# Kernel optimization log

Hardware: AMD Instinct MI355X
Metric: run time of the kernel (lower is better)

Reference implementation:

```python
import jax, jax.numpy as jnp
import numpy as np


def softmax_kernel(data, projection, is_query, eps=1e-4):
    # data: [b,h,n,d], projection: [m,d]
    d = data.shape[-1]
    data_normalizer = d ** -0.25
    ratio = projection.shape[0] ** -0.5
    data_dash = jnp.einsum('bhnd,md->bhnm', data_normalizer * data, projection)
    diag_data = (data ** 2).sum(axis=-1) * 0.5 * (data_normalizer ** 2)  # [b,h,n]
    diag_data = diag_data[..., None]
    if is_query:
        m = jnp.max(data_dash, axis=-1, keepdims=True)  # per-query max
    else:
        m = jnp.max(data_dash)  # global max over all keys
    return ratio * (jnp.exp(data_dash - diag_data - m) + eps)


def linear_attention(q, k, v):
    # q,k: [b,h,n,m] feature maps; v: [b,h,n,e]
    D_inv = 1.0 / jnp.einsum('bhnm,bhm->bhn', q, k.sum(axis=-2))
    context = jnp.einsum('bhnm,bhne->bhme', k, v)
    return jnp.einsum('bhme,bhnm,bhn->bhne', context, q, D_inv)


def setup_inputs() -> dict:
    key = jax.random.key(0)
    k1, k2, k3, k4 = jax.random.split(key, 4)
    B, H, N, D, M = 4, 16, 4096, 64, 256
    # gaussian orthogonal random matrix (scaling=0): 4 orthogonal DxD blocks,
    # rows rescaled by norms of gaussian rows
    blocks = []
    kk = k4
    for _ in range(M // D):
        kk, sub = jax.random.split(kk)
        g = jax.random.normal(sub, (D, D), dtype=jnp.float32)
        qmat, _ = jnp.linalg.qr(g)
        blocks.append(qmat.T)
    final = jnp.concatenate(blocks, axis=0)  # [M, D]
    kk, sub = jax.random.split(kk)
    multiplier = jnp.linalg.norm(jax.random.normal(sub, (M, D), dtype=jnp.float32), axis=1)
    proj = multiplier[:, None] * final
    return {
        'q': jax.random.normal(k1, (B, H, N, D), dtype=jnp.float32),
        'k': jax.random.normal(k2, (B, H, N, D), dtype=jnp.float32),
        'v': jax.random.normal(k3, (B, H, N, D), dtype=jnp.float32),
        'projection': proj,
    }


def reference(q, k, v, projection):
    q_prime = softmax_kernel(q, projection, is_query=True)
    k_prime = softmax_kernel(k, projection, is_query=False)
    return linear_attention(q_prime, k_prime, v)
```

## Files before the change

### kernel.cpp

```cpp
#include <hip/hip_runtime.h>
#include <hip/hip_bf16.h>


#define BH    64
#define NSEQ  4096
#define DD    64
#define MM    256
#define DN    0.35355339059327373f
#define RATIO 0.0625f
#define EPS   1e-4f
#define NSEG  8

#define CTX_OFF  0
#define KSUM_OFF (BH*MM*DD)
#define VSUM_OFF (KSUM_OFF + BH*MM)
#define MG_OFF   (VSUM_OFF + BH*DD)
#define CTX_SLICE (BH*MM*DD)

typedef __attribute__((ext_vector_type(8)))  short bf16x8;
typedef __attribute__((ext_vector_type(16))) float f32x16;

#define MFMA(a,b,c) __builtin_amdgcn_mfma_f32_32x32x16_bf16((a),(b),(c),0,0,0)
#define PATROW(r,h) ((((r)&3) + 8*((r)>>2)) + 4*(h))

__device__ __forceinline__ unsigned pkbf(float lo, float hi) {
    union { __hip_bfloat162 b2; unsigned u; } cvt;
    cvt.b2 = __float22bfloat162_rn(make_float2(lo, hi));
    return cvt.u;
}
__device__ __forceinline__ bf16x8 hi8(const float* x) {
    union { unsigned w[4]; bf16x8 v; } r;
    r.w[0] = pkbf(x[0], x[1]);
    r.w[1] = pkbf(x[2], x[3]);
    r.w[2] = pkbf(x[4], x[5]);
    r.w[3] = pkbf(x[6], x[7]);
    return r.v;
}
__device__ __forceinline__ unsigned short f2bf(float x) {
    unsigned u = __float_as_uint(x);
    return (unsigned short)((u + 0x7fffu + ((u >> 16) & 1u)) >> 16);
}
__device__ __forceinline__ unsigned ford(float f) {
    unsigned u = __float_as_uint(f);
    return (u & 0x80000000u) ? ~u : (u | 0x80000000u);
}
__device__ __forceinline__ float ford_inv(unsigned u) {
    return (u & 0x80000000u) ? __uint_as_float(u & 0x7fffffffu) : __uint_as_float(~u);
}
template<int BASE>
__device__ __forceinline__ bf16x8 repack8(const f32x16& a, int h) {
    unsigned X0 = pkbf(a[BASE+0], a[BASE+1]);
    unsigned X1 = pkbf(a[BASE+2], a[BASE+3]);
    unsigned Y0 = pkbf(a[BASE+4], a[BASE+5]);
    unsigned Y1 = pkbf(a[BASE+6], a[BASE+7]);
    unsigned tX0 = (unsigned)__shfl_xor((int)X0, 32);
    unsigned tX1 = (unsigned)__shfl_xor((int)X1, 32);
    unsigned tY0 = (unsigned)__shfl_xor((int)Y0, 32);
    unsigned tY1 = (unsigned)__shfl_xor((int)Y1, 32);
    union { unsigned w[4]; bf16x8 v; } r;
    r.w[0] = h ? tY0 : X0;
    r.w[1] = h ? tY1 : X1;
    r.w[2] = h ? Y0 : tX0;
    r.w[3] = h ? Y1 : tX1;
    return r.v;
}

__global__ __launch_bounds__(512, 2)
void keys_kernel(const float* __restrict__ kg, const float* __restrict__ vg,
                 const float* __restrict__ pg, float* __restrict__ ws,
                 float* __restrict__ outp)
{
    __shared__ __align__(16) short kf[2][64*64];
    __shared__ __align__(16) short vT[2][64*64];
    __shared__ float diagl[2][64];
    __shared__ float vswr[8][64];

    const int tid  = threadIdx.x;
    const int wv   = tid >> 6;
    const int lane = tid & 63;
    const int l31  = lane & 31;
    const int h    = lane >> 5;
    const int bh   = blockIdx.x >> 3;
    const int seg  = blockIdx.x & 7;

    const int kn = tid >> 3, kdg = tid & 7;
    const int ve = tid & 63, vnr = tid >> 6;

    bf16x8 pBh[4];
    {
        const int m = 32*wv + l31;
#pragma unroll
        for (int ks = 0; ks < 4; ++ks) {
            const int d0 = 16*ks + 8*h;
            float x[8];
            *(float4*)&x[0] = *(const float4*)(pg + m*64 + d0);
            *(float4*)&x[4] = *(const float4*)(pg + m*64 + d0 + 4);
#pragma unroll
            for (int i = 0; i < 8; ++i) x[i] *= DN;
            pBh[ks] = hi8(x);
        }
    }

    f32x16 cacc0, cacc1;
#pragma unroll
    for (int i = 0; i < 16; ++i) { cacc0[i] = 0.f; cacc1[i] = 0.f; }
    float ksacc = 0.f, mloc = -3e38f, vsacc = 0.f;

    float kx[8], vx[8];

    auto loads = [&](int ch) {
        const size_t kb = ((size_t)(bh*NSEQ + seg*512 + ch*64 + kn)) * 64 + kdg*8;
        *(float4*)&kx[0] = *(const float4*)(kg + kb);
        *(float4*)&kx[4] = *(const float4*)(kg + kb + 4);
        const size_t vb = ((size_t)(bh*NSEQ + seg*512 + ch*64 + vnr*8)) * 64 + ve;
#pragma unroll
        for (int j = 0; j < 8; ++j) vx[j] = vg[vb + (size_t)j*64];
    };

    auto stage_write = [&](int b) {
        float ss = 0.f;
#pragma unroll
        for (int i = 0; i < 8; ++i) ss = fmaf(kx[i], kx[i], ss);
        ss += __shfl_xor(ss, 1); ss += __shfl_xor(ss, 2); ss += __shfl_xor(ss, 4);
        if (kdg == 0) diagl[b][kn] = ss * 0.0625f;
        *(bf16x8*)&kf[b][kdg*512 + ((kn*8) ^ (kdg*8))] = hi8(kx);
#pragma unroll
        for (int j = 0; j < 8; ++j) vsacc += vx[j];
        *(bf16x8*)&vT[b][ve*64 + ((vnr*8) ^ (8*(ve & 7)))] = hi8(vx);
    };

    auto sgemm = [&](int b, f32x16& r0, f32x16& r1) {
#pragma unroll
        for (int i = 0; i < 16; ++i) { r0[i] = 0.f; r1[i] = 0.f; }
#pragma unroll
        for (int ks = 0; ks < 4; ++ks) {
            const int dg = ks*2 + h;
            const int ofs = dg*512 + ((l31*8) ^ (dg*8));
            bf16x8 a0 = *(const bf16x8*)&kf[b][ofs];
            bf16x8 a1 = *(const bf16x8*)&kf[b][ofs + 256];
            r0 = MFMA(a0, pBh[ks], r0);
            r1 = MFMA(a1, pBh[ks], r1);
        }
    };

    loads(0);
    stage_write(0);
    __syncthreads();

    for (int ch = 0; ch < 8; ++ch) {
        const int bc = ch & 1, bn = bc ^ 1;
        if (ch < 7) loads(ch + 1);

        f32x16 s0, s1;
        __builtin_amdgcn_s_setprio(1);
        sgemm(bc, s0, s1);
        __builtin_amdgcn_s_setprio(0);

        {
            float kp = 0.f;
#pragma unroll
            for (int g = 0; g < 4; ++g) {
                const float4 dq0 = *(const float4*)&diagl[bc][8*g + 4*h];
                const float4 dq1 = *(const float4*)&diagl[bc][32 + 8*g + 4*h];
                const float d0[4] = {dq0.x, dq0.y, dq0.z, dq0.w};
                const float d1[4] = {dq1.x, dq1.y, dq1.z, dq1.w};
#pragma unroll
                for (int j = 0; j < 4; ++j) {
                    const int r = 4*g + j;
                    mloc = fmaxf(mloc, s0[r]);
                    const float w0 = __expf(s0[r] - d0[j]);
                    s0[r] = w0; kp += w0;
                    mloc = fmaxf(mloc, s1[r]);
                    const float w1 = __expf(s1[r] - d1[j]);
                    s1[r] = w1; kp += w1;
                }
            }
            ksacc += kp;
        }
        bf16x8 wfr[4];
        wfr[0] = repack8<0>(s0, h);
        wfr[1] = repack8<8>(s0, h);
        wfr[2] = repack8<0>(s1, h);
        wfr[3] = repack8<8>(s1, h);

        __builtin_amdgcn_s_setprio(1);
#pragma unroll
        for (int ks = 0; ks < 4; ++ks) {
            const int nb = 16*ks + 8*h;
            const int sw = 8*(l31 & 7);
            bf16x8 b0 = *(const bf16x8*)&vT[bc][l31*64      + (nb ^ sw)];
            bf16x8 b1 = *(const bf16x8*)&vT[bc][(l31+32)*64 + (nb ^ sw)];
            cacc0 = MFMA(wfr[ks], b0, cacc0);
            cacc1 = MFMA(wfr[ks], b1, cacc1);
        }
        __builtin_amdgcn_s_setprio(0);

        if (ch < 7) stage_write(bn);
        __syncthreads();
    }

    ksacc += __shfl_xor(ksacc, 32);
    if (h == 0) atomicAdd(&ws[KSUM_OFF + bh*MM + 32*wv + l31], ksacc);

#pragma unroll
    for (int m = 1; m <= 32; m <<= 1) mloc = fmaxf(mloc, __shfl_xor(mloc, m));
    if (lane == 0) atomicMax((unsigned*)&ws[MG_OFF], ford(mloc));

    {
        float* cb = outp + (size_t)(seg*BH + bh) * (MM*DD);
#pragma unroll
        for (int r = 0; r < 16; ++r) {
            const int m = 32*wv + PATROW(r, h);
            cb[m*64 + l31]      = cacc0[r];
            cb[m*64 + l31 + 32] = cacc1[r];
        }
    }

    vswr[wv][lane] = vsacc;
    __syncthreads();
    if (tid < 64) {
        float s = 0.f;
#pragma unroll
        for (int w = 0; w < 8; ++w) s += vswr[w][tid];
        atomicAdd(&ws[VSUM_OFF + bh*DD + tid], s);
    }
}

__global__ __launch_bounds__(512)
void reduce_kernel(const float* __restrict__ outp, float* __restrict__ ws)
{
    const int idx = blockIdx.x * 512 + threadIdx.x;
    const float4* o4 = (const float4*)outp;
    float4 s = o4[idx];
#pragma unroll
    for (int sl = 1; sl < NSEG; ++sl) {
        float4 t = o4[sl*(CTX_SLICE/4) + idx];
        s.x += t.x; s.y += t.y; s.z += t.z; s.w += t.w;
    }
    ((float4*)(ws + CTX_OFF))[idx] = s;
}

__global__ __launch_bounds__(512, 2)
void query_kernel(const float* __restrict__ qg, const float* __restrict__ pg,
                  const float* __restrict__ ws, float* __restrict__ out)
{
    __shared__ __align__(16) short pfh[MM*DD];
    __shared__ __align__(16) short ctxb[32*64*8];
    __shared__ float ksuml[MM];
    __shared__ float ctxsuml[DD];
    __shared__ float ksumsuml;
    __shared__ float epsl[8][32];
    __shared__ float denl[8][32];

    const int tid  = threadIdx.x;
    const int wv   = tid >> 6;
    const int lane = tid & 63;
    const int l31  = lane & 31;
    const int h    = lane >> 5;
    const int bh   = blockIdx.x >> 3;
    const int seg  = blockIdx.x & 7;

    const float mg = ford_inv(*(const unsigned*)&ws[MG_OFF]);
    const float cs = RATIO * __expf(-mg);
    const float ce = RATIO * EPS;

    if (tid < DD) ctxsuml[tid] = 0.f;
    if (tid == 0) ksumsuml = 0.f;
    __syncthreads();

    {
        const int m = tid >> 1, dh = tid & 1;
#pragma unroll
        for (int b = 0; b < 4; ++b) {
            const int d0 = dh*32 + b*8;
            float x[8];
            *(float4*)&x[0] = *(const float4*)(pg + m*64 + d0);
            *(float4*)&x[4] = *(const float4*)(pg + m*64 + d0 + 4);
#pragma unroll
            for (int i = 0; i < 8; ++i) x[i] *= DN;
            const int g = ((m>>5)*4 + (d0>>4))*2 + ((d0>>3)&1);
            *(bf16x8*)&pfh[(g*32 + (m&31))*8] = hi8(x);
        }
    }
#pragma unroll
    for (int it = 0; it < 4; ++it) {
        const int gid = it*512 + tid;
        const int g = gid >> 6, e = gid & 63;
        const int mb = (g>>1)*16 + (g&1)*8;
        const float vs = ws[VSUM_OFF + bh*DD + e];
        float part = 0.f;
        float xv[8];
#pragma unroll
        for (int j = 0; j < 8; ++j) {
            xv[j] = cs*ws[CTX_OFF + (size_t)bh*(MM*DD) + (mb+j)*64 + e] + ce*vs;
            part += xv[j];
        }
        *(bf16x8*)&ctxb[(g*64 + e)*8] = hi8(xv);
        atomicAdd(&ctxsuml[e], part);
    }
    if (tid < 256) {
        const float kt = cs*ws[KSUM_OFF + bh*MM + tid] + ce*(float)NSEQ;
        ksuml[tid] = kt;
        atomicAdd(&ksumsuml, kt);
    }
    __syncthreads();

    const float cs0 = ctxsuml[l31];
    const float cs1 = ctxsuml[l31 + 32];
    const float kss = ksumsuml;

    for (int ch = 0; ch < 2; ++ch) {
        const int rown = seg*512 + ch*256 + wv*32;
        const size_t gn = (size_t)(bh*NSEQ + rown + l31);

        bf16x8 qbh[4];
        float ss = 0.f;
#pragma unroll
        for (int ks = 0; ks < 4; ++ks) {
            const int d0 = 16*ks + 8*h;
            float x[8];
            *(float4*)&x[0] = *(const float4*)(qg + gn*64 + d0);
            *(float4*)&x[4] = *(const float4*)(qg + gn*64 + d0 + 4);
#pragma unroll
            for (int i = 0; i < 8; ++i) ss = fmaf(x[i], x[i], ss);
            qbh[ks] = hi8(x);
        }
        const float diag = (ss + __shfl_xor(ss, 32)) * 0.0625f;

        f32x16 n0, n1;
#pragma unroll
        for (int i = 0; i < 16; ++i) { n0[i] = 0.f; n1[i] = 0.f; }
        float den = 0.f, mx = -3e38f;
#pragma unroll
        for (int mt = 0; mt < 8; ++mt) {
            f32x16 s;
#pragma unroll
            for (int i = 0; i < 16; ++i) s[i] = 0.f;
#pragma unroll
            for (int ks = 0; ks < 4; ++ks) {
                const int g = (mt*4 + ks)*2 + h;
                bf16x8 ah = *(const bf16x8*)&pfh[(g*32 + l31)*8];
                s = MFMA(ah, qbh[ks], s);
            }
#pragma unroll
            for (int r = 0; r < 16; ++r) mx = fmaxf(mx, s[r]);
#pragma unroll
            for (int r = 0; r < 16; ++r) {
                const float u = __expf(s[r] - diag);
                s[r] = u;
                den = fmaf(u, ksuml[mt*32 + PATROW(r, h)], den);
            }
            bf16x8 t0 = repack8<0>(s, h);
            bf16x8 t1 = repack8<8>(s, h);
            const int g0 = 4*mt + h, g1 = 4*mt + 2 + h;
            n0 = MFMA(t0, *(const bf16x8*)&ctxb[(g0*64 + l31)*8],      n0);
            n1 = MFMA(t0, *(const bf16x8*)&ctxb[(g0*64 + l31 + 32)*8], n1);
            n0 = MFMA(t1, *(const bf16x8*)&ctxb[(g1*64 + l31)*8],      n0);
            n1 = MFMA(t1, *(const bf16x8*)&ctxb[(g1*64 + l31 + 32)*8], n1);
        }

        mx  = fmaxf(mx, __shfl_xor(mx, 32));
        den += __shfl_xor(den, 32);
        const float epsp = EPS * __expf(mx);
        const float denf = den + epsp * kss;
        if (h == 0) { epsl[wv][l31] = epsp; denl[wv][l31] = denf; }
        asm volatile("s_waitcnt lgkmcnt(0)" ::: "memory");

#pragma unroll
        for (int r = 0; r < 16; ++r) {
            const int nn = PATROW(r, h);
            const float e1  = epsl[wv][nn];
            const float rdn = 1.0f / denl[wv][nn];
            float* op = out + ((size_t)(bh*NSEQ + rown + nn))*64;
            op[l31]      = (n0[r] + e1*cs0) * rdn;
            op[l31 + 32] = (n1[r] + e1*cs1) * rdn;
        }
    }
}

extern "C" void kernel_launch(void* const* d_in, const int* in_sizes, int n_in,
                              void* d_out, int out_size, void* d_ws, size_t ws_size,
                              hipStream_t stream)
{
    const float* q = (const float*)d_in[0];
    const float* k = (const float*)d_in[1];
    const float* v = (const float*)d_in[2];
    const float* p = (const float*)d_in[3];
    float* ws  = (float*)d_ws;
    float* out = (float*)d_out;

    (void)hipMemsetAsync((void*)(ws + KSUM_OFF),
                         0, (size_t)(BH*MM + BH*DD + 4) * sizeof(float), stream);
    keys_kernel<<<dim3(512), dim3(512), 0, stream>>>(k, v, p, ws, out);
    reduce_kernel<<<dim3(512), dim3(512), 0, stream>>>(out, ws);
    query_kernel<<<dim3(512), dim3(512), 0, stream>>>(q, p, ws, out);
}
```

Baseline: 141.6 us.

## Load K/V fragments directly from global into registers, drop LDS staging and barriers

The keys kernel no longer stages K and V chunks through double-buffered shared memory. Each wave now loads its own K rows and V columns straight from global memory into MFMA fragment registers and computes the diagonal norm with a cross-half shuffle. The per-row diagonal subtraction is folded into the score accumulator through an extra MFMA with a split-bf16 hi/lo encoding. Removing LDS traffic and __syncthreads is meant to cut staging overhead, but every wave redundantly re-reads the same K and V tiles from global/L2, and the software prefetch overlap is lost.

```diff
diff --git a/kernel.cpp b/kernel.cpp
--- a/kernel.cpp
+++ b/kernel.cpp
@@ -70,11 +70,6 @@
                  const float* __restrict__ pg, float* __restrict__ ws,
                  float* __restrict__ outp)
 {
-    __shared__ __align__(16) short kf[2][64*64];
-    __shared__ __align__(16) short vT[2][64*64];
-    __shared__ float diagl[2][64];
-    __shared__ float vswr[8][64];
-
     const int tid  = threadIdx.x;
     const int wv   = tid >> 6;
     const int lane = tid & 63;
@@ -83,9 +78,6 @@
     const int bh   = blockIdx.x >> 3;
     const int seg  = blockIdx.x & 7;
 
-    const int kn = tid >> 3, kdg = tid & 7;
-    const int ve = tid & 63, vnr = tid >> 6;
-
     bf16x8 pBh[4];
     {
         const int m = 32*wv + l31;
@@ -101,102 +93,109 @@
         }
     }
 
+    union { unsigned w[4]; bf16x8 v; } dBu;
+    dBu.w[0] = h ? 0u : 0xBF80BF80u;
+    dBu.w[1] = 0u; dBu.w[2] = 0u; dBu.w[3] = 0u;
+    const bf16x8 dB = dBu.v;
+
     f32x16 cacc0, cacc1;
 #pragma unroll
     for (int i = 0; i < 16; ++i) { cacc0[i] = 0.f; cacc1[i] = 0.f; }
-    float ksacc = 0.f, mloc = -3e38f, vsacc = 0.f;
-
-    float kx[8], vx[8];
-
-    auto loads = [&](int ch) {
-        const size_t kb = ((size_t)(bh*NSEQ + seg*512 + ch*64 + kn)) * 64 + kdg*8;
-        *(float4*)&kx[0] = *(const float4*)(kg + kb);
-        *(float4*)&kx[4] = *(const float4*)(kg + kb + 4);
-        const size_t vb = ((size_t)(bh*NSEQ + seg*512 + ch*64 + vnr*8)) * 64 + ve;
-#pragma unroll
-        for (int j = 0; j < 8; ++j) vx[j] = vg[vb + (size_t)j*64];
-    };
-
-    auto stage_write = [&](int b) {
-        float ss = 0.f;
-#pragma unroll
-        for (int i = 0; i < 8; ++i) ss = fmaf(kx[i], kx[i], ss);
-        ss += __shfl_xor(ss, 1); ss += __shfl_xor(ss, 2); ss += __shfl_xor(ss, 4);
-        if (kdg == 0) diagl[b][kn] = ss * 0.0625f;
-        *(bf16x8*)&kf[b][kdg*512 + ((kn*8) ^ (kdg*8))] = hi8(kx);
-#pragma unroll
-        for (int j = 0; j < 8; ++j) vsacc += vx[j];
-        *(bf16x8*)&vT[b][ve*64 + ((vnr*8) ^ (8*(ve & 7)))] = hi8(vx);
-    };
-
-    auto sgemm = [&](int b, f32x16& r0, f32x16& r1) {
-#pragma unroll
-        for (int i = 0; i < 16; ++i) { r0[i] = 0.f; r1[i] = 0.f; }
+    float ksacc = 0.f, mloc = -3e38f, vs0 = 0.f, vs1 = 0.f;
+
+    for (int ch = 0; ch < 8; ++ch) {
+        const int rowb = bh*NSEQ + seg*512 + ch*64;
+
+        bf16x8 ka0[4], ka1[4];
+        float ss0 = 0.f, ss1 = 0.f;
 #pragma unroll
         for (int ks = 0; ks < 4; ++ks) {
-            const int dg = ks*2 + h;
-            const int ofs = dg*512 + ((l31*8) ^ (dg*8));
-            bf16x8 a0 = *(const bf16x8*)&kf[b][ofs];
-            bf16x8 a1 = *(const bf16x8*)&kf[b][ofs + 256];
-            r0 = MFMA(a0, pBh[ks], r0);
-            r1 = MFMA(a1, pBh[ks], r1);
-        }
-    };
-
-    loads(0);
-    stage_write(0);
-    __syncthreads();
-
-    for (int ch = 0; ch < 8; ++ch) {
-        const int bc = ch & 1, bn = bc ^ 1;
-        if (ch < 7) loads(ch + 1);
+            const size_t a0 = ((size_t)(rowb + l31)) * 64 + 16*ks + 8*h;
+            const size_t a1 = ((size_t)(rowb + l31 + 32)) * 64 + 16*ks + 8*h;
+            float x0[8], x1[8];
+            *(float4*)&x0[0] = *(const float4*)(kg + a0);
+            *(float4*)&x0[4] = *(const float4*)(kg + a0 + 4);
+            *(float4*)&x1[0] = *(const float4*)(kg + a1);
+            *(float4*)&x1[4] = *(const float4*)(kg + a1 + 4);
+#pragma unroll
+            for (int i = 0; i < 8; ++i) {
+                ss0 = fmaf(x0[i], x0[i], ss0);
+                ss1 = fmaf(x1[i], x1[i], ss1);
+            }
+            ka0[ks] = hi8(x0);
+            ka1[ks] = hi8(x1);
+        }
+        const float diag0 = (ss0 + __shfl_xor(ss0, 32)) * 0.0625f;
+        const float diag1 = (ss1 + __shfl_xor(ss1, 32)) * 0.0625f;
 
         f32x16 s0, s1;
-        __builtin_amdgcn_s_setprio(1);
-        sgemm(bc, s0, s1);
-        __builtin_amdgcn_s_setprio(0);
+#pragma unroll
+        for (int i = 0; i < 16; ++i) { s0[i] = 0.f; s1[i] = 0.f; }
+#pragma unroll
+        for (int ks = 0; ks < 4; ++ks) {
+            s0 = MFMA(ka0[ks], pBh[ks], s0);
+            s1 = MFMA(ka1[ks], pBh[ks], s1);
+        }
+
+        bf16x8 vb0[4], vb1[4];
+#pragma unroll
+        for (int kss = 0; kss < 4; ++kss) {
+            const size_t vbse = ((size_t)(rowb + 16*kss + 8*h)) * 64;
+            float y0[8], y1[8];
+#pragma unroll
+            for (int j = 0; j < 8; ++j) {
+                y0[j] = vg[vbse + (size_t)j*64 + l31];
+                y1[j] = vg[vbse + (size_t)j*64 + l31 + 32];
+            }
+#pragma unroll
+            for (int j = 0; j < 8; ++j) { vs0 += y0[j]; vs1 += y1[j]; }
+            vb0[kss] = hi8(y0);
+            vb1[kss] = hi8(y1);
+        }
+
+#pragma unroll
+        for (int r = 0; r < 16; ++r) {
+            mloc = fmaxf(mloc, s0[r]);
+            mloc = fmaxf(mloc, s1[r]);
+        }
+
+        {
+            const float dh0 = __uint_as_float((unsigned)f2bf(diag0) << 16);
+            const float dh1 = __uint_as_float((unsigned)f2bf(diag1) << 16);
+            union { unsigned w[4]; bf16x8 v; } dA0, dA1;
+            dA0.w[0] = h ? 0u : pkbf(diag0, diag0 - dh0);
+            dA1.w[0] = h ? 0u : pkbf(diag1, diag1 - dh1);
+            dA0.w[1] = 0u; dA0.w[2] = 0u; dA0.w[3] = 0u;
+            dA1.w[1] = 0u; dA1.w[2] = 0u; dA1.w[3] = 0u;
+            s0 = MFMA(dA0.v, dB, s0);
+            s1 = MFMA(dA1.v, dB, s1);
+        }
 
         {
             float kp = 0.f;
 #pragma unroll
-            for (int g = 0; g < 4; ++g) {
-                const float4 dq0 = *(const float4*)&diagl[bc][8*g + 4*h];
-                const float4 dq1 = *(const float4*)&diagl[bc][32 + 8*g + 4*h];
-                const float d0[4] = {dq0.x, dq0.y, dq0.z, dq0.w};
-                const float d1[4] = {dq1.x, dq1.y, dq1.z, dq1.w};
-#pragma unroll
-                for (int j = 0; j < 4; ++j) {
-                    const int r = 4*g + j;
-                    mloc = fmaxf(mloc, s0[r]);
-                    const float w0 = __expf(s0[r] - d0[j]);
-                    s0[r] = w0; kp += w0;
-                    mloc = fmaxf(mloc, s1[r]);
-                    const float w1 = __expf(s1[r] - d1[j]);
-                    s1[r] = w1; kp += w1;
-                }
+            for (int r = 0; r < 16; ++r) {
+                const float w0 = __expf(s0[r]); s0[r] = w0; kp += w0;
+                const float w1 = __expf(s1[r]); s1[r] = w1; kp += w1;
             }
             ksacc += kp;
         }
-        bf16x8 wfr[4];
-        wfr[0] = repack8<0>(s0, h);
-        wfr[1] = repack8<8>(s0, h);
-        wfr[2] = repack8<0>(s1, h);
-        wfr[3] = repack8<8>(s1, h);
-
-        __builtin_amdgcn_s_setprio(1);
-#pragma unroll
-        for (int ks = 0; ks < 4; ++ks) {
-            const int nb = 16*ks + 8*h;
-            const int sw = 8*(l31 & 7);
-            bf16x8 b0 = *(const bf16x8*)&vT[bc][l31*64      + (nb ^ sw)];
-            bf16x8 b1 = *(const bf16x8*)&vT[bc][(l31+32)*64 + (nb ^ sw)];
-            cacc0 = MFMA(wfr[ks], b0, cacc0);
-            cacc1 = MFMA(wfr[ks], b1, cacc1);
-        }
-        __builtin_amdgcn_s_setprio(0);
-
-        if (ch < 7) stage_write(bn);
-        __syncthreads();
+
+        {
+            bf16x8 t;
+            t = repack8<0>(s0, h);
+            cacc0 = MFMA(t, vb0[0], cacc0);
+            cacc1 = MFMA(t, vb1[0], cacc1);
+            t = repack8<8>(s0, h);
+            cacc0 = MFMA(t, vb0[1], cacc0);
+            cacc1 = MFMA(t, vb1[1], cacc1);
+            t = repack8<0>(s1, h);
+            cacc0 = MFMA(t, vb0[2], cacc0);
+            cacc1 = MFMA(t, vb1[2], cacc1);
+            t = repack8<8>(s1, h);
+            cacc0 = MFMA(t, vb0[3], cacc0);
+            cacc1 = MFMA(t, vb1[3], cacc1);
+        }
     }
 
     ksacc += __shfl_xor(ksacc, 32);
@@ -216,13 +215,11 @@
         }
     }
 
-    vswr[wv][lane] = vsacc;
-    __syncthreads();
-    if (tid < 64) {
-        float s = 0.f;
-#pragma unroll
-        for (int w = 0; w < 8; ++w) s += vswr[w][tid];
-        atomicAdd(&ws[VSUM_OFF + bh*DD + tid], s);
+    vs0 += __shfl_xor(vs0, 32);
+    vs1 += __shfl_xor(vs1, 32);
+    if (wv == 0 && h == 0) {
+        atomicAdd(&ws[VSUM_OFF + bh*DD + l31],      vs0);
+        atomicAdd(&ws[VSUM_OFF + bh*DD + l31 + 32], vs1);
     }
 }
 
```

Measured after the change: 181.5 us. +28.1%, slower.

## Warp-specialize keys kernel with dedicated producer waves for K/V staging

Applied to the files above, without the earlier changes.

Adds two producer wavefronts to the keys kernel. They load K and V from global memory, compute the diagonal terms and V sums, and write bf16 tiles into double-buffered shared memory. The eight compute waves now only run the MFMA chain, with raw s_barrier plus lgkmcnt waits for synchronisation. This is meant to hide global-load latency behind the MFMA work without consuming compute-wave registers. In exchange, launch bounds drop to one block per CU at 640 threads, so occupancy falls, and the producer waves carry large register arrays.

```diff
diff --git a/kernel.cpp b/kernel.cpp
--- a/kernel.cpp
+++ b/kernel.cpp
@@ -22,6 +22,7 @@
 
 #define MFMA(a,b,c) __builtin_amdgcn_mfma_f32_32x32x16_bf16((a),(b),(c),0,0,0)
 #define PATROW(r,h) ((((r)&3) + 8*((r)>>2)) + 4*(h))
+#define BARRIER() asm volatile("s_waitcnt lgkmcnt(0)\n\ts_barrier" ::: "memory")
 
 __device__ __forceinline__ unsigned pkbf(float lo, float hi) {
     union { __hip_bfloat162 b2; unsigned u; } cvt;
@@ -35,10 +36,6 @@
     r.w[2] = pkbf(x[4], x[5]);
     r.w[3] = pkbf(x[6], x[7]);
     return r.v;
-}
-__device__ __forceinline__ unsigned short f2bf(float x) {
-    unsigned u = __float_as_uint(x);
-    return (unsigned short)((u + 0x7fffu + ((u >> 16) & 1u)) >> 16);
 }
 __device__ __forceinline__ unsigned ford(float f) {
     unsigned u = __float_as_uint(f);
@@ -65,7 +62,7 @@
     return r.v;
 }
 
-__global__ __launch_bounds__(512, 2)
+__global__ __launch_bounds__(640, 1)
 void keys_kernel(const float* __restrict__ kg, const float* __restrict__ vg,
                  const float* __restrict__ pg, float* __restrict__ ws,
                  float* __restrict__ outp)
@@ -73,156 +70,171 @@
     __shared__ __align__(16) short kf[2][64*64];
     __shared__ __align__(16) short vT[2][64*64];
     __shared__ float diagl[2][64];
-    __shared__ float vswr[8][64];
 
     const int tid  = threadIdx.x;
     const int wv   = tid >> 6;
     const int lane = tid & 63;
-    const int l31  = lane & 31;
-    const int h    = lane >> 5;
     const int bh   = blockIdx.x >> 3;
     const int seg  = blockIdx.x & 7;
 
-    const int kn = tid >> 3, kdg = tid & 7;
-    const int ve = tid & 63, vnr = tid >> 6;
-
-    bf16x8 pBh[4];
-    {
-        const int m = 32*wv + l31;
-#pragma unroll
-        for (int ks = 0; ks < 4; ++ks) {
-            const int d0 = 16*ks + 8*h;
-            float x[8];
-            *(float4*)&x[0] = *(const float4*)(pg + m*64 + d0);
-            *(float4*)&x[4] = *(const float4*)(pg + m*64 + d0 + 4);
-#pragma unroll
-            for (int i = 0; i < 8; ++i) x[i] *= DN;
-            pBh[ks] = hi8(x);
-        }
-    }
-
-    f32x16 cacc0, cacc1;
-#pragma unroll
-    for (int i = 0; i < 16; ++i) { cacc0[i] = 0.f; cacc1[i] = 0.f; }
-    float ksacc = 0.f, mloc = -3e38f, vsacc = 0.f;
-
-    float kx[8], vx[8];
-
-    auto loads = [&](int ch) {
-        const size_t kb = ((size_t)(bh*NSEQ + seg*512 + ch*64 + kn)) * 64 + kdg*8;
-        *(float4*)&kx[0] = *(const float4*)(kg + kb);
-        *(float4*)&kx[4] = *(const float4*)(kg + kb + 4);
-        const size_t vb = ((size_t)(bh*NSEQ + seg*512 + ch*64 + vnr*8)) * 64 + ve;
-#pragma unroll
-        for (int j = 0; j < 8; ++j) vx[j] = vg[vb + (size_t)j*64];
-    };
-
-    auto stage_write = [&](int b) {
-        float ss = 0.f;
-#pragma unroll
-        for (int i = 0; i < 8; ++i) ss = fmaf(kx[i], kx[i], ss);
-        ss += __shfl_xor(ss, 1); ss += __shfl_xor(ss, 2); ss += __shfl_xor(ss, 4);
-        if (kdg == 0) diagl[b][kn] = ss * 0.0625f;
-        *(bf16x8*)&kf[b][kdg*512 + ((kn*8) ^ (kdg*8))] = hi8(kx);
-#pragma unroll
-        for (int j = 0; j < 8; ++j) vsacc += vx[j];
-        *(bf16x8*)&vT[b][ve*64 + ((vnr*8) ^ (8*(ve & 7)))] = hi8(vx);
-    };
-
-    auto sgemm = [&](int b, f32x16& r0, f32x16& r1) {
-#pragma unroll
-        for (int i = 0; i < 16; ++i) { r0[i] = 0.f; r1[i] = 0.f; }
-#pragma unroll
-        for (int ks = 0; ks < 4; ++ks) {
-            const int dg = ks*2 + h;
-            const int ofs = dg*512 + ((l31*8) ^ (dg*8));
-            bf16x8 a0 = *(const bf16x8*)&kf[b][ofs];
-            bf16x8 a1 = *(const bf16x8*)&kf[b][ofs + 256];
-            r0 = MFMA(a0, pBh[ks], r0);
-            r1 = MFMA(a1, pBh[ks], r1);
-        }
-    };
-
-    loads(0);
-    stage_write(0);
-    __syncthreads();
-
-    for (int ch = 0; ch < 8; ++ch) {
-        const int bc = ch & 1, bn = bc ^ 1;
-        if (ch < 7) loads(ch + 1);
-
-        f32x16 s0, s1;
-        __builtin_amdgcn_s_setprio(1);
-        sgemm(bc, s0, s1);
-        __builtin_amdgcn_s_setprio(0);
-
+    if (wv < 8) {
+        const int l31 = lane & 31;
+        const int h   = lane >> 5;
+
+        bf16x8 pBh[4];
         {
-            float kp = 0.f;
+            const int m = 32*wv + l31;
+#pragma unroll
+            for (int ks = 0; ks < 4; ++ks) {
+                const int d0 = 16*ks + 8*h;
+                float x[8];
+                *(float4*)&x[0] = *(const float4*)(pg + m*64 + d0);
+                *(float4*)&x[4] = *(const float4*)(pg + m*64 + d0 + 4);
+#pragma unroll
+                for (int i = 0; i < 8; ++i) x[i] *= DN;
+                pBh[ks] = hi8(x);
+            }
+        }
+
+        f32x16 cacc0, cacc1;
+#pragma unroll
+        for (int i = 0; i < 16; ++i) { cacc0[i] = 0.f; cacc1[i] = 0.f; }
+        float ksacc = 0.f, mloc = -3e38f;
+
+        BARRIER();
+
+        for (int ch = 0; ch < 8; ++ch) {
+            const int bc = ch & 1;
+
+            f32x16 s0, s1;
+#pragma unroll
+            for (int i = 0; i < 16; ++i) { s0[i] = 0.f; s1[i] = 0.f; }
+            __builtin_amdgcn_s_setprio(1);
+#pragma unroll
+            for (int ks = 0; ks < 4; ++ks) {
+                const int dg = ks*2 + h;
+                const int ofs = dg*512 + ((l31*8) ^ (dg*8));
+                bf16x8 a0 = *(const bf16x8*)&kf[bc][ofs];
+                bf16x8 a1 = *(const bf16x8*)&kf[bc][ofs + 256];
+                s0 = MFMA(a0, pBh[ks], s0);
+                s1 = MFMA(a1, pBh[ks], s1);
+            }
+            __builtin_amdgcn_s_setprio(0);
+
+            {
+                float kp = 0.f;
+#pragma unroll
+                for (int g = 0; g < 4; ++g) {
+                    const float4 dq0 = *(const float4*)&diagl[bc][8*g + 4*h];
+                    const float4 dq1 = *(const float4*)&diagl[bc][32 + 8*g + 4*h];
+                    const float d0[4] = {dq0.x, dq0.y, dq0.z, dq0.w};
+                    const float d1[4] = {dq1.x, dq1.y, dq1.z, dq1.w};
+#pragma unroll
+                    for (int j = 0; j < 4; ++j) {
+                        const int r = 4*g + j;
+                        mloc = fmaxf(mloc, s0[r]);
+                        const float w0 = __expf(s0[r] - d0[j]);
+                        s0[r] = w0; kp += w0;
+                        mloc = fmaxf(mloc, s1[r]);
+                        const float w1 = __expf(s1[r] - d1[j]);
+                        s1[r] = w1; kp += w1;
+                    }
+                }
+                ksacc += kp;
+            }
+            bf16x8 wfr[4];
+            wfr[0] = repack8<0>(s0, h);
+            wfr[1] = repack8<8>(s0, h);
+            wfr[2] = repack8<0>(s1, h);
+            wfr[3] = repack8<8>(s1, h);
+
+            __builtin_amdgcn_s_setprio(1);
+#pragma unroll
+            for (int ks = 0; ks < 4; ++ks) {
+                const int nb = 16*ks + 8*h;
+                const int sw = 8*(l31 & 7);
+                bf16x8 b0 = *(const bf16x8*)&vT[bc][l31*64      + (nb ^ sw)];
+                bf16x8 b1 = *(const bf16x8*)&vT[bc][(l31+32)*64 + (nb ^ sw)];
+                cacc0 = MFMA(wfr[ks], b0, cacc0);
+                cacc1 = MFMA(wfr[ks], b1, cacc1);
+            }
+            __builtin_amdgcn_s_setprio(0);
+
+            BARRIER();
+        }
+
+        ksacc += __shfl_xor(ksacc, 32);
+        if (h == 0) atomicAdd(&ws[KSUM_OFF + bh*MM + 32*wv + l31], ksacc);
+
+#pragma unroll
+        for (int m = 1; m <= 32; m <<= 1) mloc = fmaxf(mloc, __shfl_xor(mloc, m));
+        if (lane == 0) atomicMax((unsigned*)&ws[MG_OFF], ford(mloc));
+
+        {
+            float* cb = outp + (size_t)(seg*BH + bh) * (MM*DD);
+#pragma unroll
+            for (int r = 0; r < 16; ++r) {
+                const int m = 32*wv + PATROW(r, h);
+                cb[m*64 + l31]      = cacc0[r];
+                cb[m*64 + l31 + 32] = cacc1[r];
+            }
+        }
+    } else {
+        const int pt  = tid - 512;
+        const int kn  = pt >> 1;
+        const int dh  = pt & 1;
+        const int ve  = pt & 63;
+        const int vo0 = (pt >> 6) * 4;
+
+        float kx[32], vx[32];
+        float vsacc = 0.f;
+
+        auto loads = [&](int ch) {
+            const int rowb = bh*NSEQ + seg*512 + ch*64;
+            const size_t kb = ((size_t)(rowb + kn))*64 + dh*32;
+#pragma unroll
+            for (int g = 0; g < 8; ++g)
+                *(float4*)&kx[4*g] = *(const float4*)(kg + kb + 4*g);
+            const size_t vb = ((size_t)(rowb + vo0*8))*64 + ve;
+#pragma unroll
+            for (int j = 0; j < 32; ++j)
+                vx[j] = vg[vb + (size_t)j*64];
+        };
+
+        auto stage_write = [&](int b) {
+            float ss = 0.f;
+#pragma unroll
+            for (int i = 0; i < 32; ++i) ss = fmaf(kx[i], kx[i], ss);
+            ss += __shfl_xor(ss, 1);
+            if (dh == 0) diagl[b][kn] = ss * 0.0625f;
 #pragma unroll
             for (int g = 0; g < 4; ++g) {
-                const float4 dq0 = *(const float4*)&diagl[bc][8*g + 4*h];
-                const float4 dq1 = *(const float4*)&diagl[bc][32 + 8*g + 4*h];
-                const float d0[4] = {dq0.x, dq0.y, dq0.z, dq0.w};
-                const float d1[4] = {dq1.x, dq1.y, dq1.z, dq1.w};
-#pragma unroll
-                for (int j = 0; j < 4; ++j) {
-                    const int r = 4*g + j;
-                    mloc = fmaxf(mloc, s0[r]);
-                    const float w0 = __expf(s0[r] - d0[j]);
-                    s0[r] = w0; kp += w0;
-                    mloc = fmaxf(mloc, s1[r]);
-                    const float w1 = __expf(s1[r] - d1[j]);
-                    s1[r] = w1; kp += w1;
-                }
-            }
-            ksacc += kp;
-        }
-        bf16x8 wfr[4];
-        wfr[0] = repack8<0>(s0, h);
-        wfr[1] = repack8<8>(s0, h);
-        wfr[2] = repack8<0>(s1, h);
-        wfr[3] = repack8<8>(s1, h);
-
-        __builtin_amdgcn_s_setprio(1);
-#pragma unroll
-        for (int ks = 0; ks < 4; ++ks) {
-            const int nb = 16*ks + 8*h;
-            const int sw = 8*(l31 & 7);
-            bf16x8 b0 = *(const bf16x8*)&vT[bc][l31*64      + (nb ^ sw)];
-            bf16x8 b1 = *(const bf16x8*)&vT[bc][(l31+32)*64 + (nb ^ sw)];
-            cacc0 = MFMA(wfr[ks], b0, cacc0);
-            cacc1 = MFMA(wfr[ks], b1, cacc1);
-        }
-        __builtin_amdgcn_s_setprio(0);
-
-        if (ch < 7) stage_write(bn);
-        __syncthreads();
-    }
-
-    ksacc += __shfl_xor(ksacc, 32);
-    if (h == 0) atomicAdd(&ws[KSUM_OFF + bh*MM + 32*wv + l31], ksacc);
-
-#pragma unroll
-    for (int m = 1; m <= 32; m <<= 1) mloc = fmaxf(mloc, __shfl_xor(mloc, m));
-    if (lane == 0) atomicMax((unsigned*)&ws[MG_OFF], ford(mloc));
-
-    {
-        float* cb = outp + (size_t)(seg*BH + bh) * (MM*DD);
-#pragma unroll
-        for (int r = 0; r < 16; ++r) {
-            const int m = 32*wv + PATROW(r, h);
-            cb[m*64 + l31]      = cacc0[r];
-            cb[m*64 + l31 + 32] = cacc1[r];
-        }
-    }
-
-    vswr[wv][lane] = vsacc;
-    __syncthreads();
-    if (tid < 64) {
-        float s = 0.f;
-#pragma unroll
-        for (int w = 0; w < 8; ++w) s += vswr[w][tid];
-        atomicAdd(&ws[VSUM_OFF + bh*DD + tid], s);
+                const int dg = 4*dh + g;
+                *(bf16x8*)&kf[b][dg*512 + ((kn*8) ^ (dg*8))] = hi8(&kx[8*g]);
+            }
+#pragma unroll
+            for (int o = 0; o < 4; ++o) {
+#pragma unroll
+                for (int j = 0; j < 8; ++j) vsacc += vx[8*o + j];
+                const int oct = vo0 + o;
+                *(bf16x8*)&vT[b][ve*64 + ((oct*8) ^ (8*(ve & 7)))] = hi8(&vx[8*o]);
+            }
+        };
+
+        loads(0);
+        stage_write(0);
+        loads(1);
+        BARRIER();
+
+        for (int ch = 0; ch < 8; ++ch) {
+            if (ch < 7) {
+                stage_write((ch + 1) & 1);
+                if (ch < 6) loads(ch + 2);
+            }
+            BARRIER();
+        }
+
+        atomicAdd(&ws[VSUM_OFF + bh*DD + ve], vsacc);
     }
 }
 
@@ -391,7 +403,7 @@
 
     (void)hipMemsetAsync((void*)(ws + KSUM_OFF),
                          0, (size_t)(BH*MM + BH*DD + 4) * sizeof(float), stream);
-    keys_kernel<<<dim3(512), dim3(512), 0, stream>>>(k, v, p, ws, out);
+    keys_kernel<<<dim3(512), dim3(640), 0, stream>>>(k, v, p, ws, out);
     reduce_kernel<<<dim3(512), dim3(512), 0, stream>>>(out, ws);
     query_kernel<<<dim3(512), dim3(512), 0, stream>>>(q, p, ws, out);
 }
```

After: 140.1 us. Within noise of the previous version (-1.1%).
